# Optimization experiments

Measured on AMD Instinct MI355X. Metric: run time of the kernel, lower is better.

Reference implementation:

```python
import jax, jax.numpy as jnp
import numpy as np

K = 3          # kernel_size
K2 = K * K     # 9
G = 8          # group
EPS = 1e-5


def _bn(x, gamma, beta, mean, var):
    # eval-mode BatchNorm over channel axis (x: (B, P))
    return gamma * (x - mean) * jax.lax.rsqrt(var + EPS) + beta


def setup_inputs() -> dict:
    key = jax.random.key(0)
    ks = jax.random.split(key, 13)
    B, C, H, W = 16, 67, 128, 128
    Pm = G * K2   # 72 main filter params
    Pr = K2       # 9 remainder filter params
    inp = {
        "x": jax.random.normal(ks[0], (B, C, H, W), jnp.float32),
        "w_main": jax.random.normal(ks[1], (Pm, C), jnp.float32) * 0.05,
        "w_gate_main": jax.random.normal(ks[2], (Pm, Pm), jnp.float32) * 0.05,
        "w_rem": jax.random.normal(ks[3], (Pr, C), jnp.float32) * 0.05,
        "w_gate_rem": jax.random.normal(ks[4], (Pr, Pr), jnp.float32) * 0.05,
        "bn_main_gamma": 1.0 + 0.1 * jax.random.normal(ks[5], (Pm,), jnp.float32),
        "bn_main_beta": 0.1 * jax.random.normal(ks[6], (Pm,), jnp.float32),
        "bn_main_mean": 0.1 * jax.random.normal(ks[7], (Pm,), jnp.float32),
        "bn_main_var": 0.75 + 0.5 * jax.random.uniform(ks[8], (Pm,), jnp.float32),
        "bn_rem_gamma": 1.0 + 0.1 * jax.random.normal(ks[9], (Pr,), jnp.float32),
        "bn_rem_beta": 0.1 * jax.random.normal(ks[10], (Pr,), jnp.float32),
        "bn_rem_mean": 0.1 * jax.random.normal(ks[11], (Pr,), jnp.float32),
        "bn_rem_var": 0.75 + 0.5 * jax.random.uniform(ks[12], (Pr,), jnp.float32),
    }
    return inp


def reference(x, w_main, w_gate_main, w_rem, w_gate_rem,
              bn_main_gamma, bn_main_beta, bn_main_mean, bn_main_var,
              bn_rem_gamma, bn_rem_beta, bn_rem_mean, bn_rem_var):
    B, C, H, W = x.shape
    main = (C // G) * G          # 64
    rem = C - main               # 3
    Cg = main // G               # 8 channels per group

    # global average pool -> (B, C)
    pooled = x.mean(axis=(2, 3))

    # --- dynamic kernel generation, main path ---
    km = pooled @ w_main.T                                   # (B, G*K2)
    km = km * jax.nn.sigmoid(km @ w_gate_main.T)             # gate
    km = _bn(km, bn_main_gamma, bn_main_beta, bn_main_mean, bn_main_var)
    km = jax.nn.softmax(km.reshape(B, G, K2), axis=-1)       # softmax over k2

    # --- dynamic kernel generation, remainder path ---
    kr = pooled @ w_rem.T                                    # (B, K2)
    kr = kr * jax.nn.sigmoid(kr @ w_gate_rem.T)
    kr = _bn(kr, bn_rem_gamma, bn_rem_beta, bn_rem_mean, bn_rem_var)
    kr = jax.nn.softmax(kr, axis=-1)                         # (B, K2)

    # --- unfold via reflect pad + shifted slices (row-major k2 order, matches F.unfold) ---
    p = K // 2
    xp = jnp.pad(x, ((0, 0), (0, 0), (p, p), (p, p)), mode='reflect')
    patches = jnp.stack([xp[:, :, i:i + H, j:j + W]
                         for i in range(K) for j in range(K)], axis=2)  # (B, C, K2, H, W)

    pm = patches[:, :main].reshape(B, G, Cg, K2, H, W)
    out_main = jnp.einsum('bgckhw,bgk->bgchw', pm, km).reshape(B, main, H, W)
    out_rem = jnp.einsum('bckhw,bk->bchw', patches[:, main:], kr)        # (B, rem, H, W)

    out = jnp.concatenate([out_main, out_rem], axis=1)
    out_high = x - out
    return out, out_high
```

## Files before the change

kernel.cpp:

```cpp
#include <hip/hip_runtime.h>
#include <hip/hip_bf16.h>
#include <math.h>

#define B_ 16
#define C_ 67
#define H_ 128
#define W_ 128
#define MAIN_ 64
#define G_ 8
#define K2_ 9
#define PM_ 72
#define PR_ 9

__global__ __launch_bounds__(256) void pool_kernel(const float* __restrict__ x,
                                                   float* __restrict__ pooled) {
    int bc = blockIdx.x;
    const float4* p4 = (const float4*)(x + (size_t)bc * (H_ * W_));
    int tid = threadIdx.x;
    float s = 0.f;
    const int n4 = H_ * W_ / 4;
    for (int i = tid; i < n4; i += 256) {
        float4 v = p4[i];
        s += (v.x + v.y) + (v.z + v.w);
    }
    for (int off = 32; off > 0; off >>= 1) s += __shfl_down(s, off, 64);
    __shared__ float red[4];
    if ((tid & 63) == 0) red[tid >> 6] = s;
    __syncthreads();
    if (tid == 0) {
        float t = (red[0] + red[1]) + (red[2] + red[3]);
        pooled[bc] = t * (1.0f / (H_ * W_));
    }
}

__global__ __launch_bounds__(128) void gen_kernel(
    const float* __restrict__ pooled,
    const float* __restrict__ w_main, const float* __restrict__ w_gate_main,
    const float* __restrict__ w_rem,  const float* __restrict__ w_gate_rem,
    const float* __restrict__ gm, const float* __restrict__ bm,
    const float* __restrict__ mm, const float* __restrict__ vm,
    const float* __restrict__ gr, const float* __restrict__ br,
    const float* __restrict__ mr, const float* __restrict__ vr,
    float* __restrict__ km_out, float* __restrict__ kr_out) {
    int b = blockIdx.x;
    int t = threadIdx.x;
    __shared__ float pl[C_];
    __shared__ float km0[PM_];
    __shared__ float kmb[PM_];
    __shared__ float kr0[PR_];
    __shared__ float krb[PR_];
    if (t < C_) pl[t] = pooled[b * C_ + t];
    __syncthreads();
    if (t < PM_) {
        float s = 0.f;
        for (int c = 0; c < C_; ++c) s += pl[c] * w_main[t * C_ + c];
        km0[t] = s;
    }
    if (t >= 96 && t < 96 + PR_) {
        int p = t - 96;
        float s = 0.f;
        for (int c = 0; c < C_; ++c) s += pl[c] * w_rem[p * C_ + c];
        kr0[p] = s;
    }
    __syncthreads();
    if (t < PM_) {
        float gsum = 0.f;
        for (int q = 0; q < PM_; ++q) gsum += km0[q] * w_gate_main[t * PM_ + q];
        float v = km0[t] * (1.f / (1.f + expf(-gsum)));
        v = gm[t] * (v - mm[t]) * rsqrtf(vm[t] + 1e-5f) + bm[t];
        kmb[t] = v;
    }
    if (t >= 96 && t < 96 + PR_) {
        int p = t - 96;
        float gsum = 0.f;
        for (int q = 0; q < PR_; ++q) gsum += kr0[q] * w_gate_rem[p * PR_ + q];
        float v = kr0[p] * (1.f / (1.f + expf(-gsum)));
        v = gr[p] * (v - mr[p]) * rsqrtf(vr[p] + 1e-5f) + br[p];
        krb[p] = v;
    }
    __syncthreads();
    if (t < PM_) {
        int base = (t / K2_) * K2_;
        float mx = -1e30f;
        for (int k = 0; k < K2_; ++k) mx = fmaxf(mx, kmb[base + k]);
        float den = 0.f;
        for (int k = 0; k < K2_; ++k) den += expf(kmb[base + k] - mx);
        km_out[b * PM_ + t] = expf(kmb[t] - mx) / den;
    }
    if (t >= 96 && t < 96 + PR_) {
        int p = t - 96;
        float mx = -1e30f;
        for (int k = 0; k < K2_; ++k) mx = fmaxf(mx, krb[k]);
        float den = 0.f;
        for (int k = 0; k < K2_; ++k) den += expf(krb[k] - mx);
        kr_out[b * PR_ + p] = expf(krb[p] - mx) / den;
    }
}

__global__ __launch_bounds__(256) void conv_kernel(const float* __restrict__ x,
                                                   const float* __restrict__ km,
                                                   const float* __restrict__ kr,
                                                   float* __restrict__ out) {
    const int b = blockIdx.z;
    const int c = blockIdx.y;
    const int t = threadIdx.x;
    const int row_in = t >> 5;
    const int t4 = t & 31;
    const int h = blockIdx.x * 8 + row_in;
    const int c0 = t4 * 4;

    const float* wp = (c < MAIN_) ? (km + ((size_t)b * G_ + (c >> 3)) * K2_)
                                  : (kr + (size_t)b * K2_);
    float k0 = wp[0], k1 = wp[1], k2 = wp[2],
          k3 = wp[3], k4 = wp[4], k5 = wp[5],
          k6 = wp[6], k7 = wp[7], k8 = wp[8];

    const float* xb = x + ((size_t)b * C_ + c) * (H_ * W_);
    const int hm = (h == 0) ? 1 : h - 1;
    const int hp = (h == H_ - 1) ? H_ - 2 : h + 1;
    const int cl = (c0 == 0) ? 1 : c0 - 1;
    const int cr = (c0 == W_ - 4) ? W_ - 2 : c0 + 4;

    const float* r0 = xb + hm * W_;
    const float* r1 = xb + (size_t)h * W_;
    const float* r2 = xb + hp * W_;

    float4 v0 = *(const float4*)(r0 + c0);
    float a0 = r0[cl], f0 = r0[cr];
    float4 v1 = *(const float4*)(r1 + c0);
    float a1 = r1[cl], f1 = r1[cr];
    float4 v2 = *(const float4*)(r2 + c0);
    float a2 = r2[cl], f2 = r2[cr];

    float4 acc;
    acc.x = k0*a0   + k1*v0.x + k2*v0.y
          + k3*a1   + k4*v1.x + k5*v1.y
          + k6*a2   + k7*v2.x + k8*v2.y;
    acc.y = k0*v0.x + k1*v0.y + k2*v0.z
          + k3*v1.x + k4*v1.y + k5*v1.z
          + k6*v2.x + k7*v2.y + k8*v2.z;
    acc.z = k0*v0.y + k1*v0.z + k2*v0.w
          + k3*v1.y + k4*v1.z + k5*v1.w
          + k6*v2.y + k7*v2.z + k8*v2.w;
    acc.w = k0*v0.z + k1*v0.w + k2*f0
          + k3*v1.z + k4*v1.w + k5*f1
          + k6*v2.z + k7*v2.w + k8*f2;

    size_t base = (((size_t)b * C_ + c) * H_ + h) * W_ + c0;
    *(float4*)(out + base) = acc;
    float4 hi;
    hi.x = v1.x - acc.x;
    hi.y = v1.y - acc.y;
    hi.z = v1.z - acc.z;
    hi.w = v1.w - acc.w;
    *(float4*)(out + base + (size_t)B_ * C_ * H_ * W_) = hi;
}

extern "C" void kernel_launch(void* const* d_in, const int* in_sizes, int n_in,
                              void* d_out, int out_size, void* d_ws, size_t ws_size,
                              hipStream_t stream) {
    const float* x           = (const float*)d_in[0];
    const float* w_main      = (const float*)d_in[1];
    const float* w_gate_main = (const float*)d_in[2];
    const float* w_rem       = (const float*)d_in[3];
    const float* w_gate_rem  = (const float*)d_in[4];
    const float* gm = (const float*)d_in[5];
    const float* bm = (const float*)d_in[6];
    const float* mm = (const float*)d_in[7];
    const float* vm = (const float*)d_in[8];
    const float* gr = (const float*)d_in[9];
    const float* br = (const float*)d_in[10];
    const float* mr = (const float*)d_in[11];
    const float* vr = (const float*)d_in[12];

    float* out = (float*)d_out;

    float* pooled = (float*)d_ws;
    float* km_ws  = pooled + B_ * C_;
    float* kr_ws  = km_ws + B_ * PM_;

    pool_kernel<<<B_ * C_, 256, 0, stream>>>(x, pooled);

    gen_kernel<<<B_, 128, 0, stream>>>(pooled, w_main, w_gate_main, w_rem, w_gate_rem,
                                       gm, bm, mm, vm, gr, br, mr, vr, km_ws, kr_ws);

    dim3 grid(H_ / 8, C_, B_);
    conv_kernel<<<grid, 256, 0, stream>>>(x, km_ws, kr_ws, out);
}
```

Baseline: 237.6 us.

## Fuse dynamic kernel generation into conv kernel, one block per (batch, channel) plane

Measured after the change: 240.9 us. No clear change (+1.4%).

```diff
diff --git a/kernel.cpp b/kernel.cpp
--- a/kernel.cpp
+++ b/kernel.cpp
@@ -1,5 +1,4 @@
 #include <hip/hip_runtime.h>
-#include <hip/hip_bf16.h>
 #include <math.h>
 
 #define B_ 16
@@ -33,127 +32,131 @@
     }
 }
 
-__global__ __launch_bounds__(128) void gen_kernel(
-    const float* __restrict__ pooled,
+__global__ __launch_bounds__(256) void conv_gen_kernel(
+    const float* __restrict__ x, const float* __restrict__ pooled,
     const float* __restrict__ w_main, const float* __restrict__ w_gate_main,
     const float* __restrict__ w_rem,  const float* __restrict__ w_gate_rem,
     const float* __restrict__ gm, const float* __restrict__ bm,
     const float* __restrict__ mm, const float* __restrict__ vm,
     const float* __restrict__ gr, const float* __restrict__ br,
     const float* __restrict__ mr, const float* __restrict__ vr,
-    float* __restrict__ km_out, float* __restrict__ kr_out) {
-    int b = blockIdx.x;
-    int t = threadIdx.x;
+    float* __restrict__ out)
+{
+    const int c = blockIdx.x;
+    const int b = blockIdx.y;
+    const int t = threadIdx.x;
+
     __shared__ float pl[C_];
-    __shared__ float km0[PM_];
-    __shared__ float kmb[PM_];
-    __shared__ float kr0[PR_];
-    __shared__ float krb[PR_];
+    __shared__ float v0s[PM_];
+    __shared__ float kb9[K2_];
+    __shared__ float wgt[K2_];
+
     if (t < C_) pl[t] = pooled[b * C_ + t];
     __syncthreads();
-    if (t < PM_) {
-        float s = 0.f;
-        for (int c = 0; c < C_; ++c) s += pl[c] * w_main[t * C_ + c];
-        km0[t] = s;
-    }
-    if (t >= 96 && t < 96 + PR_) {
-        int p = t - 96;
-        float s = 0.f;
-        for (int c = 0; c < C_; ++c) s += pl[c] * w_rem[p * C_ + c];
-        kr0[p] = s;
+
+    if (c < MAIN_) {
+        const int g = c >> 3;
+        if (t < PM_) {
+            float s = 0.f;
+            for (int i = 0; i < C_; ++i) s += pl[i] * w_main[t * C_ + i];
+            v0s[t] = s;
+        }
+        __syncthreads();
+        if (t < K2_) {
+            int row = g * K2_ + t;
+            float gsum = 0.f;
+            for (int q = 0; q < PM_; ++q) gsum += v0s[q] * w_gate_main[row * PM_ + q];
+            float v = v0s[row] * (1.f / (1.f + expf(-gsum)));
+            v = gm[row] * (v - mm[row]) * rsqrtf(vm[row] + 1e-5f) + bm[row];
+            kb9[t] = v;
+        }
+        __syncthreads();
+        if (t < K2_) {
+            float mx = -1e30f;
+            for (int k = 0; k < K2_; ++k) mx = fmaxf(mx, kb9[k]);
+            float den = 0.f;
+            for (int k = 0; k < K2_; ++k) den += expf(kb9[k] - mx);
+            wgt[t] = expf(kb9[t] - mx) / den;
+        }
+    } else {
+        if (t < PR_) {
+            float s = 0.f;
+            for (int i = 0; i < C_; ++i) s += pl[i] * w_rem[t * C_ + i];
+            v0s[t] = s;
+        }
+        __syncthreads();
+        if (t < PR_) {
+            float gsum = 0.f;
+            for (int q = 0; q < PR_; ++q) gsum += v0s[q] * w_gate_rem[t * PR_ + q];
+            float v = v0s[t] * (1.f / (1.f + expf(-gsum)));
+            v = gr[t] * (v - mr[t]) * rsqrtf(vr[t] + 1e-5f) + br[t];
+            kb9[t] = v;
+        }
+        __syncthreads();
+        if (t < PR_) {
+            float mx = -1e30f;
+            for (int k = 0; k < K2_; ++k) mx = fmaxf(mx, kb9[k]);
+            float den = 0.f;
+            for (int k = 0; k < K2_; ++k) den += expf(kb9[k] - mx);
+            wgt[t] = expf(kb9[t] - mx) / den;
+        }
     }
     __syncthreads();
-    if (t < PM_) {
-        float gsum = 0.f;
-        for (int q = 0; q < PM_; ++q) gsum += km0[q] * w_gate_main[t * PM_ + q];
-        float v = km0[t] * (1.f / (1.f + expf(-gsum)));
-        v = gm[t] * (v - mm[t]) * rsqrtf(vm[t] + 1e-5f) + bm[t];
-        kmb[t] = v;
+
+    const float k0 = wgt[0], k1 = wgt[1], k2 = wgt[2],
+                k3 = wgt[3], k4 = wgt[4], k5 = wgt[5],
+                k6 = wgt[6], k7 = wgt[7], k8 = wgt[8];
+
+    const size_t bc = (size_t)b * C_ + c;
+    const float* xb = x + bc * (H_ * W_);
+    float* ob = out + bc * (H_ * W_);
+    float* oh = ob + (size_t)B_ * C_ * H_ * W_;
+
+    #pragma unroll
+    for (int it = 0; it < 16; ++it) {
+        int task = it * 256 + t;
+        int h  = task >> 5;
+        int c0 = (task & 31) * 4;
+
+        int hm = (h == 0) ? 1 : h - 1;
+        int hp = (h == H_ - 1) ? H_ - 2 : h + 1;
+        int cl = (c0 == 0) ? 1 : c0 - 1;
+        int cr = (c0 == W_ - 4) ? W_ - 2 : c0 + 4;
+
+        const float* r0 = xb + hm * W_;
+        const float* r1 = xb + (size_t)h * W_;
+        const float* r2 = xb + hp * W_;
+
+        float4 v0 = *(const float4*)(r0 + c0);
+        float a0 = r0[cl], f0 = r0[cr];
+        float4 v1 = *(const float4*)(r1 + c0);
+        float a1 = r1[cl], f1 = r1[cr];
+        float4 v2 = *(const float4*)(r2 + c0);
+        float a2 = r2[cl], f2 = r2[cr];
+
+        float4 acc;
+        acc.x = k0*a0   + k1*v0.x + k2*v0.y
+              + k3*a1   + k4*v1.x + k5*v1.y
+              + k6*a2   + k7*v2.x + k8*v2.y;
+        acc.y = k0*v0.x + k1*v0.y + k2*v0.z
+              + k3*v1.x + k4*v1.y + k5*v1.z
+              + k6*v2.x + k7*v2.y + k8*v2.z;
+        acc.z = k0*v0.y + k1*v0.z + k2*v0.w
+              + k3*v1.y + k4*v1.z + k5*v1.w
+              + k6*v2.y + k7*v2.z + k8*v2.w;
+        acc.w = k0*v0.z + k1*v0.w + k2*f0
+              + k3*v1.z + k4*v1.w + k5*f1
+              + k6*v2.z + k7*v2.w + k8*f2;
+
+        size_t off = (size_t)h * W_ + c0;
+        *(float4*)(ob + off) = acc;
+        float4 hi;
+        hi.x = v1.x - acc.x;
+        hi.y = v1.y - acc.y;
+        hi.z = v1.z - acc.z;
+        hi.w = v1.w - acc.w;
+        *(float4*)(oh + off) = hi;
     }
-    if (t >= 96 && t < 96 + PR_) {
-        int p = t - 96;
-        float gsum = 0.f;
-        for (int q = 0; q < PR_; ++q) gsum += kr0[q] * w_gate_rem[p * PR_ + q];
-        float v = kr0[p] * (1.f / (1.f + expf(-gsum)));
-        v = gr[p] * (v - mr[p]) * rsqrtf(vr[p] + 1e-5f) + br[p];
-        krb[p] = v;
-    }
-    __syncthreads();
-    if (t < PM_) {
-        int base = (t / K2_) * K2_;
-        float mx = -1e30f;
-        for (int k = 0; k < K2_; ++k) mx = fmaxf(mx, kmb[base + k]);
-        float den = 0.f;
-        for (int k = 0; k < K2_; ++k) den += expf(kmb[base + k] - mx);
-        km_out[b * PM_ + t] = expf(kmb[t] - mx) / den;
-    }
-    if (t >= 96 && t < 96 + PR_) {
-        int p = t - 96;
-        float mx = -1e30f;
-        for (int k = 0; k < K2_; ++k) mx = fmaxf(mx, krb[k]);
-        float den = 0.f;
-        for (int k = 0; k < K2_; ++k) den += expf(krb[k] - mx);
-        kr_out[b * PR_ + p] = expf(krb[p] - mx) / den;
-    }
-}
-
-__global__ __launch_bounds__(256) void conv_kernel(const float* __restrict__ x,
-                                                   const float* __restrict__ km,
-                                                   const float* __restrict__ kr,
-                                                   float* __restrict__ out) {
-    const int b = blockIdx.z;
-    const int c = blockIdx.y;
-    const int t = threadIdx.x;
-    const int row_in = t >> 5;
-    const int t4 = t & 31;
-    const int h = blockIdx.x * 8 + row_in;
-    const int c0 = t4 * 4;
-
-    const float* wp = (c < MAIN_) ? (km + ((size_t)b * G_ + (c >> 3)) * K2_)
-                                  : (kr + (size_t)b * K2_);
-    float k0 = wp[0], k1 = wp[1], k2 = wp[2],
-          k3 = wp[3], k4 = wp[4], k5 = wp[5],
-          k6 = wp[6], k7 = wp[7], k8 = wp[8];
-
-    const float* xb = x + ((size_t)b * C_ + c) * (H_ * W_);
-    const int hm = (h == 0) ? 1 : h - 1;
-    const int hp = (h == H_ - 1) ? H_ - 2 : h + 1;
-    const int cl = (c0 == 0) ? 1 : c0 - 1;
-    const int cr = (c0 == W_ - 4) ? W_ - 2 : c0 + 4;
-
-    const float* r0 = xb + hm * W_;
-    const float* r1 = xb + (size_t)h * W_;
-    const float* r2 = xb + hp * W_;
-
-    float4 v0 = *(const float4*)(r0 + c0);
-    float a0 = r0[cl], f0 = r0[cr];
-    float4 v1 = *(const float4*)(r1 + c0);
-    float a1 = r1[cl], f1 = r1[cr];
-    float4 v2 = *(const float4*)(r2 + c0);
-    float a2 = r2[cl], f2 = r2[cr];
-
-    float4 acc;
-    acc.x = k0*a0   + k1*v0.x + k2*v0.y
-          + k3*a1   + k4*v1.x + k5*v1.y
-          + k6*a2   + k7*v2.x + k8*v2.y;
-    acc.y = k0*v0.x + k1*v0.y + k2*v0.z
-          + k3*v1.x + k4*v1.y + k5*v1.z
-          + k6*v2.x + k7*v2.y + k8*v2.z;
-    acc.z = k0*v0.y + k1*v0.z + k2*v0.w
-          + k3*v1.y + k4*v1.z + k5*v1.w
-          + k6*v2.y + k7*v2.z + k8*v2.w;
-    acc.w = k0*v0.z + k1*v0.w + k2*f0
-          + k3*v1.z + k4*v1.w + k5*f1
-          + k6*v2.z + k7*v2.w + k8*f2;
-
-    size_t base = (((size_t)b * C_ + c) * H_ + h) * W_ + c0;
-    *(float4*)(out + base) = acc;
-    float4 hi;
-    hi.x = v1.x - acc.x;
-    hi.y = v1.y - acc.y;
-    hi.z = v1.z - acc.z;
-    hi.w = v1.w - acc.w;
-    *(float4*)(out + base + (size_t)B_ * C_ * H_ * W_) = hi;
 }
 
 extern "C" void kernel_launch(void* const* d_in, const int* in_sizes, int n_in,
@@ -174,16 +177,12 @@
     const float* vr = (const float*)d_in[12];
 
     float* out = (float*)d_out;
-
     float* pooled = (float*)d_ws;
-    float* km_ws  = pooled + B_ * C_;
-    float* kr_ws  = km_ws + B_ * PM_;
 
     pool_kernel<<<B_ * C_, 256, 0, stream>>>(x, pooled);
 
-    gen_kernel<<<B_, 128, 0, stream>>>(pooled, w_main, w_gate_main, w_rem, w_gate_rem,
-                                       gm, bm, mm, vm, gr, br, mr, vr, km_ws, kr_ws);
-
-    dim3 grid(H_ / 8, C_, B_);
-    conv_kernel<<<grid, 256, 0, stream>>>(x, km_ws, kr_ws, out);
+    dim3 grid(C_, B_);
+    conv_gen_kernel<<<grid, 256, 0, stream>>>(x, pooled,
+                                              w_main, w_gate_main, w_rem, w_gate_rem,
+                                              gm, bm, mm, vm, gr, br, mr, vr, out);
 }
```
